# Kernel tuning notes

Measured on AMD Instinct MI355X. Metric: run time of the kernel, lower is better.

## Reference

```python
import jax, jax.numpy as jnp
import numpy as np

EPS_LN = 1e-5  # eqx.nn.LayerNorm default eps
DT_EPS = 1e-4  # softplus(dt) + 0.0001 in the module

H = 256  # hidden size
S = 256  # state size
B = 32
T = 4096


def setup_inputs() -> dict:
    key = jax.random.key(0)
    ks = jax.random.split(key, 8)
    sc = 1.0 / np.sqrt(H)
    return {
        "x": jax.random.normal(ks[0], (B, T, H), jnp.float32),
        "state0": jnp.zeros((B, S), jnp.float32),
        "in_to_state": jax.random.normal(ks[1], (S, H), jnp.float32) * sc,
        "state_to_hidden": jax.random.normal(ks[2], (H, S), jnp.float32) * sc,
        "direct": jax.random.normal(ks[3], (H,), jnp.float32) * sc,
        "a_diag": jax.random.normal(ks[4], (S,), jnp.float32),
        "g_diag": jax.random.normal(ks[5], (S,), jnp.float32),
        "dt": jax.random.normal(ks[6], (S,), jnp.float32) * 0.5 - 2.0,  # small timesteps
        "norm_w": jnp.ones((H,), jnp.float32),
        "norm_b": jnp.zeros((H,), jnp.float32),
        "out_w": jax.random.normal(ks[7], (H, H), jnp.float32) * sc,
        "out_b": jnp.zeros((H,), jnp.float32),
    }


def reference(x, state0, in_to_state, state_to_hidden, direct, a_diag, g_diag,
              dt, norm_w, norm_b, out_w, out_b):
    # Discretized diagonal oscillator coefficients (input-independent)
    dt_s = jax.nn.softplus(dt) + DT_EPS            # [S]
    omega = a_diag * dt_s                          # [S]
    decay = jnp.exp(-jax.nn.softplus(g_diag) * dt_s)
    decay = decay * decay                          # damped=True
    coeff = decay * jnp.cos(omega)                 # [S]

    # LayerNorm over feature dim (per-timestep, matching eqx.nn.LayerNorm)
    mu = jnp.mean(x, axis=-1, keepdims=True)
    var = jnp.var(x, axis=-1, keepdims=True)
    x_norm = (x - mu) * jax.lax.rsqrt(var + EPS_LN) * norm_w + norm_b  # [B,T,H]

    # Input injection: in_to_state @ x_norm for every timestep
    u = jnp.einsum("sh,bth->bts", in_to_state, x_norm)  # [B,T,S]

    # Diagonal linear recurrence: s_t = coeff * s_{t-1} + u_t
    def step(s, u_t):
        s = coeff * s + u_t
        return s, s

    u_t_major = jnp.swapaxes(u, 0, 1)                    # [T,B,S]
    final_state, states = jax.lax.scan(step, state0, u_t_major)
    states = jnp.swapaxes(states, 0, 1)                  # [B,T,S]

    # Readout + skip + gelu + out projection + residual
    mixed = jnp.einsum("hs,bts->bth", state_to_hidden, states) + direct * x_norm
    mixed = jax.nn.gelu(mixed)
    y = x + jnp.einsum("oh,bth->bto", out_w, mixed) + out_b
    return y, final_state
```

## Files before the change

kernel.cpp:

```cpp
#include <hip/hip_runtime.h>
#include <hip/hip_bf16.h>
#include <cstdint>
#include <cstddef>


typedef __bf16 bf16x8 __attribute__((ext_vector_type(8)));
typedef __bf16 bf16x4 __attribute__((ext_vector_type(4)));
typedef float  f32x4  __attribute__((ext_vector_type(4)));
typedef unsigned int u32x4 __attribute__((ext_vector_type(4)));

#define BB 32
#define TT 4096
#define HH 256
#define SS 256
#define MTOT (BB*TT)
#define NCHUNK 64
#define CLEN 64
#define NT 8

__global__ void prep_kernel(const float* __restrict__ w1, const float* __restrict__ w2,
                            const float* __restrict__ w3,
                            __bf16* __restrict__ w1b, __bf16* __restrict__ w2b,
                            __bf16* __restrict__ w3b,
                            const float* __restrict__ a_diag, const float* __restrict__ g_diag,
                            const float* __restrict__ dt,
                            float* __restrict__ coeff, float* __restrict__ cL) {
    int i = blockIdx.x * 256 + threadIdx.x;
    w1b[i] = (__bf16)w1[i];
    w2b[i] = (__bf16)w2[i];
    w3b[i] = (__bf16)w3[i];
    if (i < SS) {
        float d = dt[i];
        float sp = (d > 20.f) ? d : log1pf(expf(d));
        float dts = sp + 1e-4f;
        float omega = a_diag[i] * dts;
        float gg = g_diag[i];
        float spg = (gg > 20.f) ? gg : log1pf(expf(gg));
        float dec = expf(-spg * dts);
        float c = dec * dec * cosf(omega);
        coeff[i] = c;
        float p = c;
        #pragma unroll
        for (int q = 0; q < 6; ++q) p = p * p;
        cL[i] = p;
    }
}

__global__ __launch_bounds__(256) void ln_kernel(const float* __restrict__ x,
                          const float* __restrict__ w, const float* __restrict__ b,
                          __bf16* __restrict__ xn) {
    int row = blockIdx.x * 4 + (threadIdx.x >> 6);
    int lane = threadIdx.x & 63;
    size_t base = (size_t)row * HH + lane * 4;
    const float4 v = *(const float4*)&x[base];
    float s  = v.x + v.y + v.z + v.w;
    float ss = v.x*v.x + v.y*v.y + v.z*v.z + v.w*v.w;
    #pragma unroll
    for (int off = 32; off; off >>= 1) {
        s  += __shfl_xor(s,  off, 64);
        ss += __shfl_xor(ss, off, 64);
    }
    float mu  = s * (1.f/256.f);
    float var = ss * (1.f/256.f) - mu*mu;
    float sc  = rsqrtf(var + 1e-5f);
    const float4 wv = *(const float4*)&w[lane*4];
    const float4 bv = *(const float4*)&b[lane*4];
    union { __bf16 h[4]; uint2 u; } pk;
    pk.h[0] = (__bf16)((v.x - mu)*sc*wv.x + bv.x);
    pk.h[1] = (__bf16)((v.y - mu)*sc*wv.y + bv.y);
    pk.h[2] = (__bf16)((v.z - mu)*sc*wv.z + bv.z);
    pk.h[3] = (__bf16)((v.w - mu)*sc*wv.w + bv.w);
    *(uint2*)&xn[base] = pk.u;
}

template<int MODE>
__global__ __launch_bounds__(512, 2) void gemm_kernel(
    const __bf16* __restrict__ W,
    const __bf16* __restrict__ X,
    void* Cout,
    const __bf16* xn_in,
    const float* __restrict__ dvec,
    const float* __restrict__ xres,
    const float* __restrict__ bias)
{
    __shared__ __bf16 Xs[64 * 256];
    __shared__ __bf16 Es[64 * 256];

    const int tid  = threadIdx.x;
    const int lane = tid & 63;
    const int wid  = tid >> 6;
    const int l15  = lane & 15, quad = lane >> 4;
    const int wn   = wid >> 1;
    const int wm   = wid & 1;

    bf16x8 Wf[4][8];
    #pragma unroll
    for (int jn = 0; jn < 4; ++jn) {
        const int n = wn * 64 + jn * 16 + l15;
        #pragma unroll
        for (int kb = 0; kb < 8; ++kb)
            Wf[jn][kb] = *(const bf16x8*)&W[(size_t)n * 256 + kb * 32 + quad * 8];
    }

    int srow[4], scol[4], sdst[4];
    #pragma unroll
    for (int j = 0; j < 4; ++j) {
        int o = wid * 256 + j * 64 + lane;
        int m = o >> 5, g = o & 31;
        srow[j] = m;
        scol[j] = g * 8;
        sdst[j] = m * 512 + ((g ^ (m & 15)) * 16);
    }

    const size_t mbase = (size_t)blockIdx.x * (64 * NT);

    u32x4 pf[4];
    #pragma unroll
    for (int j = 0; j < 4; ++j)
        pf[j] = *(const u32x4*)&X[(mbase + srow[j]) * 256 + scol[j]];
    #pragma unroll
    for (int j = 0; j < 4; ++j)
        *(u32x4*)((char*)Xs + sdst[j]) = pf[j];
    __syncthreads();
    #pragma unroll
    for (int j = 0; j < 4; ++j)
        pf[j] = *(const u32x4*)&X[(mbase + 64 + srow[j]) * 256 + scol[j]];

    const int mrow0 = wm * 32 + l15;
    const int hrow  = tid >> 5;
    const int nc    = tid & 31;

    for (int it = 0; it < NT; ++it) {
        const size_t mt0 = mbase + (size_t)it * 64;

        f32x4 acc[2][4] = {};
        #pragma unroll
        for (int kb = 0; kb < 8; ++kb) {
            bf16x8 xf[2];
            #pragma unroll
            for (int im = 0; im < 2; ++im) {
                int m = mrow0 + im * 16;
                xf[im] = *(const bf16x8*)((char*)Xs + m * 512 + (((kb * 4 + quad) ^ l15) * 16));
            }
            #pragma unroll
            for (int jn = 0; jn < 4; ++jn)
                #pragma unroll
                for (int im = 0; im < 2; ++im)
                    acc[im][jn] = __builtin_amdgcn_mfma_f32_16x16x32_bf16(
                        Wf[jn][kb], xf[im], acc[im][jn], 0, 0, 0);
        }
        __syncthreads();

        if (it + 1 < NT) {
            #pragma unroll
            for (int j = 0; j < 4; ++j)
                *(u32x4*)((char*)Xs + sdst[j]) = pf[j];
        }
        #pragma unroll
        for (int im = 0; im < 2; ++im) {
            const int m = mrow0 + im * 16;
            #pragma unroll
            for (int jn = 0; jn < 4; ++jn) {
                const int gn = wn * 16 + jn * 4 + quad;
                bf16x4 pk;
                #pragma unroll
                for (int r = 0; r < 4; ++r) pk[r] = (__bf16)acc[im][jn][r];
                *(bf16x4*)((char*)Es + m * 512 + ((gn ^ (l15 << 2)) * 8)) = pk;
            }
        }
        __syncthreads();

        if (it + 2 < NT) {
            #pragma unroll
            for (int j = 0; j < 4; ++j)
                pf[j] = *(const u32x4*)&X[(mt0 + 128 + srow[j]) * 256 + scol[j]];
        }

        #pragma unroll
        for (int r = 0; r < 4; ++r) {
            const int m = r * 16 + hrow;
            bf16x8 ev = *(const bf16x8*)((char*)Es + m * 512 + (((nc * 2) ^ (hrow << 2)) * 8));
            const size_t gidx = (mt0 + m) * 256 + nc * 8;
            if (MODE == 0) {
                *(bf16x8*)((__bf16*)Cout + gidx) = ev;
            } else if (MODE == 1) {
                bf16x8 xv = *(const bf16x8*)&xn_in[gidx];
                f32x4 d0 = *(const f32x4*)&dvec[nc * 8];
                f32x4 d1 = *(const f32x4*)&dvec[nc * 8 + 4];
                bf16x8 pk;
                #pragma unroll
                for (int j = 0; j < 8; ++j) {
                    float dj = (j < 4) ? d0[j] : d1[j - 4];
                    float t = (float)ev[j] + dj * (float)xv[j];
                    float th = tanhf(0.7978845608028654f * (t + 0.044715f * t * t * t));
                    pk[j] = (__bf16)(0.5f * t * (1.0f + th));
                }
                *(bf16x8*)((__bf16*)Cout + gidx) = pk;
            } else {
                f32x4 x0 = *(const f32x4*)&xres[gidx];
                f32x4 x1 = *(const f32x4*)&xres[gidx + 4];
                f32x4 b0 = *(const f32x4*)&bias[nc * 8];
                f32x4 b1 = *(const f32x4*)&bias[nc * 8 + 4];
                f32x4 y0, y1;
                #pragma unroll
                for (int j = 0; j < 4; ++j) {
                    y0[j] = x0[j] + (float)ev[j]     + b0[j];
                    y1[j] = x1[j] + (float)ev[j + 4] + b1[j];
                }
                *(f32x4*)((float*)Cout + gidx)     = y0;
                *(f32x4*)((float*)Cout + gidx + 4) = y1;
            }
        }
    }
}

__global__ __launch_bounds__(256) void scan_carries(const __bf16* __restrict__ u,
                             const float* __restrict__ coeff,
                             const float* __restrict__ state0, float* __restrict__ carry) {
    int ch = blockIdx.x, b = blockIdx.y, s = threadIdx.x;
    float c = coeff[s];
    float st = (ch == 0) ? state0[b * SS + s] : 0.f;
    size_t base = ((size_t)b * TT + (size_t)ch * CLEN) * SS + s;
    #pragma unroll 8
    for (int i = 0; i < CLEN; ++i)
        st = c * st + (float)u[base + (size_t)i * SS];
    carry[(b * NCHUNK + ch) * SS + s] = st;
}

__global__ __launch_bounds__(256) void scan_prefix(float* carry, const float* __restrict__ cL,
                            float* __restrict__ fs_out) {
    int b = blockIdx.x, s = threadIdx.x;
    float cl = cL[s];
    float P = 0.f;
    for (int j = 0; j < NCHUNK; ++j) {
        int idx = (b * NCHUNK + j) * SS + s;
        P = cl * P + carry[idx];
        carry[idx] = P;
    }
    fs_out[b * SS + s] = P;
}

__global__ __launch_bounds__(256) void scan_apply(__bf16* u, const float* __restrict__ coeff,
                           const float* __restrict__ state0,
                           const float* __restrict__ carry) {
    int ch = blockIdx.x, b = blockIdx.y, s = threadIdx.x;
    float c = coeff[s];
    float st = (ch == 0) ? state0[b * SS + s]
                         : carry[(b * NCHUNK + ch - 1) * SS + s];
    size_t base = ((size_t)b * TT + (size_t)ch * CLEN) * SS + s;
    #pragma unroll 8
    for (int i = 0; i < CLEN; ++i) {
        st = c * st + (float)u[base + (size_t)i * SS];
        u[base + (size_t)i * SS] = (__bf16)st;
    }
}

extern "C" void kernel_launch(void* const* d_in, const int* in_sizes, int n_in,
                              void* d_out, int out_size, void* d_ws, size_t ws_size,
                              hipStream_t stream) {
    const float* x      = (const float*)d_in[0];
    const float* state0 = (const float*)d_in[1];
    const float* w1     = (const float*)d_in[2];
    const float* w2     = (const float*)d_in[3];
    const float* direct = (const float*)d_in[4];
    const float* a_diag = (const float*)d_in[5];
    const float* g_diag = (const float*)d_in[6];
    const float* dt     = (const float*)d_in[7];
    const float* norm_w = (const float*)d_in[8];
    const float* norm_b = (const float*)d_in[9];
    const float* w3     = (const float*)d_in[10];
    const float* out_b  = (const float*)d_in[11];

    char* ws = (char*)d_ws;
    const size_t MH2 = (size_t)MTOT * HH * 2;
    __bf16* xn    = (__bf16*)(ws);
    __bf16* u     = (__bf16*)(ws + MH2);
    __bf16* w1b   = (__bf16*)(ws + 2*MH2);
    __bf16* w2b   = (__bf16*)(ws + 2*MH2 + 131072);
    __bf16* w3b   = (__bf16*)(ws + 2*MH2 + 262144);
    float*  coeff = (float*)(ws + 2*MH2 + 393216);
    float*  cL    = (float*)(ws + 2*MH2 + 394240);
    float*  carry = (float*)(ws + 2*MH2 + 395264);

    float* y_out  = (float*)d_out;
    float* fs_out = (float*)d_out + (size_t)MTOT * HH;

    prep_kernel<<<256, 256, 0, stream>>>(w1, w2, w3, w1b, w2b, w3b,
                                         a_diag, g_diag, dt, coeff, cL);
    ln_kernel<<<MTOT/4, 256, 0, stream>>>(x, norm_w, norm_b, xn);
    gemm_kernel<0><<<256, 512, 0, stream>>>(w1b, xn, u, nullptr, nullptr, nullptr, nullptr);
    scan_carries<<<dim3(NCHUNK, BB), 256, 0, stream>>>(u, coeff, state0, carry);
    scan_prefix<<<BB, 256, 0, stream>>>(carry, cL, fs_out);
    scan_apply<<<dim3(NCHUNK, BB), 256, 0, stream>>>(u, coeff, state0, carry);
    gemm_kernel<1><<<256, 512, 0, stream>>>(w2b, u, xn, xn, direct, nullptr, nullptr);
    gemm_kernel<2><<<256, 512, 0, stream>>>(w3b, xn, y_out, nullptr, nullptr, x, out_b);
}
```

Measured before the change: 430.1 us.

## Fuse chunked scan carries and apply into the GEMM kernels

```diff
diff --git a/kernel.cpp b/kernel.cpp
--- a/kernel.cpp
+++ b/kernel.cpp
@@ -15,7 +15,6 @@
 #define SS 256
 #define MTOT (BB*TT)
 #define NCHUNK 64
-#define CLEN 64
 #define NT 8
 
 __global__ void prep_kernel(const float* __restrict__ w1, const float* __restrict__ w2,
@@ -73,77 +72,141 @@
     *(uint2*)&xn[base] = pk.u;
 }
 
+__device__ __forceinline__ void scan_xs_tile(__bf16* Xs, int tid, float c, float& st) {
+    const int gb = tid >> 3, bo = (tid & 7) << 1;
+    #pragma unroll
+    for (int g4 = 0; g4 < 4; ++g4) {
+        float v[8];
+        #pragma unroll
+        for (int r = 0; r < 8; ++r) {
+            const int m = g4 * 8 + r;
+            v[r] = (float)*(const __bf16*)((const char*)Xs + m * 512 + (((gb ^ (m & 15)) << 4) | bo));
+        }
+        __bf16 w[8];
+        #pragma unroll
+        for (int r = 0; r < 8; ++r) { st = c * st + v[r]; w[r] = (__bf16)st; }
+        #pragma unroll
+        for (int r = 0; r < 8; ++r) {
+            const int m = g4 * 8 + r;
+            *(__bf16*)((char*)Xs + m * 512 + (((gb ^ (m & 15)) << 4) | bo)) = w[r];
+        }
+    }
+}
+
+__device__ __forceinline__ void scan_es_carry(const __bf16* Es, int tid, float c, float& st) {
+    const int gb = tid >> 2, bo = (tid & 3) << 1;
+    #pragma unroll
+    for (int g4 = 0; g4 < 4; ++g4) {
+        float v[8];
+        #pragma unroll
+        for (int r = 0; r < 8; ++r) {
+            const int m = g4 * 8 + r;
+            v[r] = (float)*(const __bf16*)((const char*)Es + m * 512 + (((gb ^ ((m & 15) << 2)) << 3) | bo));
+        }
+        #pragma unroll
+        for (int r = 0; r < 8; ++r) st = c * st + v[r];
+    }
+}
+
 template<int MODE>
-__global__ __launch_bounds__(512, 2) void gemm_kernel(
+__global__ __launch_bounds__(512, 4) void gemm_kernel(
     const __bf16* __restrict__ W,
     const __bf16* __restrict__ X,
     void* Cout,
     const __bf16* xn_in,
     const float* __restrict__ dvec,
     const float* __restrict__ xres,
-    const float* __restrict__ bias)
+    const float* __restrict__ bias,
+    const float* __restrict__ coeff,
+    const float* __restrict__ state0,
+    float* carry)
 {
-    __shared__ __bf16 Xs[64 * 256];
-    __shared__ __bf16 Es[64 * 256];
+    __shared__ __bf16 Xs[32 * 256];
+    __shared__ __bf16 Es[32 * 256];
 
     const int tid  = threadIdx.x;
     const int lane = tid & 63;
     const int wid  = tid >> 6;
     const int l15  = lane & 15, quad = lane >> 4;
-    const int wn   = wid >> 1;
-    const int wm   = wid & 1;
-
-    bf16x8 Wf[4][8];
-    #pragma unroll
-    for (int jn = 0; jn < 4; ++jn) {
-        const int n = wn * 64 + jn * 16 + l15;
+
+    bf16x8 Wf[2][8];
+    #pragma unroll
+    for (int jn = 0; jn < 2; ++jn) {
+        const int n = wid * 32 + jn * 16 + l15;
         #pragma unroll
         for (int kb = 0; kb < 8; ++kb)
             Wf[jn][kb] = *(const bf16x8*)&W[(size_t)n * 256 + kb * 32 + quad * 8];
     }
 
-    int srow[4], scol[4], sdst[4];
-    #pragma unroll
-    for (int j = 0; j < 4; ++j) {
-        int o = wid * 256 + j * 64 + lane;
-        int m = o >> 5, g = o & 31;
+    const int bxi = blockIdx.x;
+    const int bb  = bxi >> 4;
+    const int chb = (bxi & 15) * 4;
+    float c_s = 0.f, s0v = 0.f, cin0 = 0.f, cin1 = 0.f, cin2 = 0.f, cin3 = 0.f;
+    if constexpr (MODE == 0) {
+        if (tid < 256) {
+            c_s = coeff[tid];
+            if (chb == 0) s0v = state0[(size_t)bb * 256 + tid];
+        }
+    }
+    if constexpr (MODE == 1) {
+        if (tid < 256) {
+            c_s = coeff[tid];
+            cin0 = (chb == 0) ? state0[(size_t)bb * 256 + tid]
+                              : carry[((size_t)bb * 64 + chb - 1) * 256 + tid];
+            cin1 = carry[((size_t)bb * 64 + chb + 0) * 256 + tid];
+            cin2 = carry[((size_t)bb * 64 + chb + 1) * 256 + tid];
+            cin3 = carry[((size_t)bb * 64 + chb + 2) * 256 + tid];
+        }
+    }
+
+    int sdst[2], srow[2];
+    const int g = tid & 31;
+    #pragma unroll
+    for (int j = 0; j < 2; ++j) {
+        const int m = j * 16 + (tid >> 5);
         srow[j] = m;
-        scol[j] = g * 8;
         sdst[j] = m * 512 + ((g ^ (m & 15)) * 16);
     }
-
-    const size_t mbase = (size_t)blockIdx.x * (64 * NT);
-
-    u32x4 pf[4];
-    #pragma unroll
-    for (int j = 0; j < 4; ++j)
-        pf[j] = *(const u32x4*)&X[(mbase + srow[j]) * 256 + scol[j]];
-    #pragma unroll
-    for (int j = 0; j < 4; ++j)
+    const int colb = g * 16;
+
+    const size_t mbase = (size_t)bxi * 256;
+    const char* Xb = (const char*)X;
+
+    u32x4 pf[2];
+    #pragma unroll
+    for (int j = 0; j < 2; ++j)
+        pf[j] = *(const u32x4*)(Xb + (mbase + srow[j]) * 512 + colb);
+    #pragma unroll
+    for (int j = 0; j < 2; ++j)
         *(u32x4*)((char*)Xs + sdst[j]) = pf[j];
     __syncthreads();
     #pragma unroll
-    for (int j = 0; j < 4; ++j)
-        pf[j] = *(const u32x4*)&X[(mbase + 64 + srow[j]) * 256 + scol[j]];
-
-    const int mrow0 = wm * 32 + l15;
-    const int hrow  = tid >> 5;
-    const int nc    = tid & 31;
+    for (int j = 0; j < 2; ++j)
+        pf[j] = *(const u32x4*)(Xb + (mbase + 32 + srow[j]) * 512 + colb);
+
+    float st  = 0.f;
+    float stc = 0.f;
+    if constexpr (MODE == 1) {
+        if (tid < 256) { st = cin0; scan_xs_tile(Xs, tid, c_s, st); }
+        __syncthreads();
+    }
+
+    const int hrow = tid >> 5;
+    const int nc   = tid & 31;
 
     for (int it = 0; it < NT; ++it) {
-        const size_t mt0 = mbase + (size_t)it * 64;
-
-        f32x4 acc[2][4] = {};
+        const size_t mt0 = mbase + (size_t)it * 32;
+
+        f32x4 acc[2][2] = {};
         #pragma unroll
         for (int kb = 0; kb < 8; ++kb) {
             bf16x8 xf[2];
             #pragma unroll
-            for (int im = 0; im < 2; ++im) {
-                int m = mrow0 + im * 16;
-                xf[im] = *(const bf16x8*)((char*)Xs + m * 512 + (((kb * 4 + quad) ^ l15) * 16));
-            }
-            #pragma unroll
-            for (int jn = 0; jn < 4; ++jn)
+            for (int im = 0; im < 2; ++im)
+                xf[im] = *(const bf16x8*)((const char*)Xs + (l15 + im * 16) * 512
+                                          + (((kb * 4 + quad) ^ l15) * 16));
+            #pragma unroll
+            for (int jn = 0; jn < 2; ++jn)
                 #pragma unroll
                 for (int im = 0; im < 2; ++im)
                     acc[im][jn] = __builtin_amdgcn_mfma_f32_16x16x32_bf16(
@@ -153,15 +216,15 @@
 
         if (it + 1 < NT) {
             #pragma unroll
-            for (int j = 0; j < 4; ++j)
+            for (int j = 0; j < 2; ++j)
                 *(u32x4*)((char*)Xs + sdst[j]) = pf[j];
         }
         #pragma unroll
         for (int im = 0; im < 2; ++im) {
-            const int m = mrow0 + im * 16;
-            #pragma unroll
-            for (int jn = 0; jn < 4; ++jn) {
-                const int gn = wn * 16 + jn * 4 + quad;
+            const int m = l15 + im * 16;
+            #pragma unroll
+            for (int jn = 0; jn < 2; ++jn) {
+                const int gn = wid * 8 + jn * 4 + quad;
                 bf16x4 pk;
                 #pragma unroll
                 for (int r = 0; r < 4; ++r) pk[r] = (__bf16)acc[im][jn][r];
@@ -172,14 +235,25 @@
 
         if (it + 2 < NT) {
             #pragma unroll
-            for (int j = 0; j < 4; ++j)
-                pf[j] = *(const u32x4*)&X[(mt0 + 128 + srow[j]) * 256 + scol[j]];
-        }
-
-        #pragma unroll
-        for (int r = 0; r < 4; ++r) {
+            for (int j = 0; j < 2; ++j)
+                pf[j] = *(const u32x4*)(Xb + (mt0 + 64 + srow[j]) * 512 + colb);
+        }
+
+        if constexpr (MODE == 1) {
+            if (it + 1 < NT && tid < 256) {
+                const int itt = it + 1;
+                if ((itt & 1) == 0) {
+                    const int k = itt >> 1;
+                    st = (k == 1) ? cin1 : (k == 2) ? cin2 : cin3;
+                }
+                scan_xs_tile(Xs, tid, c_s, st);
+            }
+        }
+
+        #pragma unroll
+        for (int r = 0; r < 2; ++r) {
             const int m = r * 16 + hrow;
-            bf16x8 ev = *(const bf16x8*)((char*)Es + m * 512 + (((nc * 2) ^ (hrow << 2)) * 8));
+            bf16x8 ev = *(const bf16x8*)((const char*)Es + m * 512 + (((nc * 2) ^ (hrow << 2)) * 8));
             const size_t gidx = (mt0 + m) * 256 + nc * 8;
             if (MODE == 0) {
                 *(bf16x8*)((__bf16*)Cout + gidx) = ev;
@@ -192,8 +266,9 @@
                 for (int j = 0; j < 8; ++j) {
                     float dj = (j < 4) ? d0[j] : d1[j - 4];
                     float t = (float)ev[j] + dj * (float)xv[j];
-                    float th = tanhf(0.7978845608028654f * (t + 0.044715f * t * t * t));
-                    pk[j] = (__bf16)(0.5f * t * (1.0f + th));
+                    float q = t + 0.044715f * t * t * t;
+                    float e = __expf(-1.5957691216057308f * q);
+                    pk[j] = (__bf16)(t * __builtin_amdgcn_rcpf(1.f + e));
                 }
                 *(bf16x8*)((__bf16*)Cout + gidx) = pk;
             } else {
@@ -211,20 +286,20 @@
                 *(f32x4*)((float*)Cout + gidx + 4) = y1;
             }
         }
-    }
-}
-
-__global__ __launch_bounds__(256) void scan_carries(const __bf16* __restrict__ u,
-                             const float* __restrict__ coeff,
-                             const float* __restrict__ state0, float* __restrict__ carry) {
-    int ch = blockIdx.x, b = blockIdx.y, s = threadIdx.x;
-    float c = coeff[s];
-    float st = (ch == 0) ? state0[b * SS + s] : 0.f;
-    size_t base = ((size_t)b * TT + (size_t)ch * CLEN) * SS + s;
-    #pragma unroll 8
-    for (int i = 0; i < CLEN; ++i)
-        st = c * st + (float)u[base + (size_t)i * SS];
-    carry[(b * NCHUNK + ch) * SS + s] = st;
+
+        if constexpr (MODE == 0) {
+            if (tid < 256) {
+                if ((it & 1) == 0) stc = (it == 0 && chb == 0) ? s0v : 0.f;
+                scan_es_carry(Es, tid, c_s, stc);
+                if ((it & 1) == 1)
+                    carry[((size_t)bb * 64 + (chb + (it >> 1))) * 256 + tid] = stc;
+            }
+        }
+
+        if constexpr (MODE == 1) {
+            if (it + 1 < NT) __syncthreads();
+        }
+    }
 }
 
 __global__ __launch_bounds__(256) void scan_prefix(float* carry, const float* __restrict__ cL,
@@ -238,21 +313,6 @@
         carry[idx] = P;
     }
     fs_out[b * SS + s] = P;
-}
-
-__global__ __launch_bounds__(256) void scan_apply(__bf16* u, const float* __restrict__ coeff,
-                           const float* __restrict__ state0,
-                           const float* __restrict__ carry) {
-    int ch = blockIdx.x, b = blockIdx.y, s = threadIdx.x;
-    float c = coeff[s];
-    float st = (ch == 0) ? state0[b * SS + s]
-                         : carry[(b * NCHUNK + ch - 1) * SS + s];
-    size_t base = ((size_t)b * TT + (size_t)ch * CLEN) * SS + s;
-    #pragma unroll 8
-    for (int i = 0; i < CLEN; ++i) {
-        st = c * st + (float)u[base + (size_t)i * SS];
-        u[base + (size_t)i * SS] = (__bf16)st;
-    }
 }
 
 extern "C" void kernel_launch(void* const* d_in, const int* in_sizes, int n_in,
@@ -288,10 +348,11 @@
     prep_kernel<<<256, 256, 0, stream>>>(w1, w2, w3, w1b, w2b, w3b,
                                          a_diag, g_diag, dt, coeff, cL);
     ln_kernel<<<MTOT/4, 256, 0, stream>>>(x, norm_w, norm_b, xn);
-    gemm_kernel<0><<<256, 512, 0, stream>>>(w1b, xn, u, nullptr, nullptr, nullptr, nullptr);
-    scan_carries<<<dim3(NCHUNK, BB), 256, 0, stream>>>(u, coeff, state0, carry);
+    gemm_kernel<0><<<512, 512, 0, stream>>>(w1b, xn, u, nullptr, nullptr, nullptr, nullptr,
+                                            coeff, state0, carry);
     scan_prefix<<<BB, 256, 0, stream>>>(carry, cL, fs_out);
-    scan_apply<<<dim3(NCHUNK, BB), 256, 0, stream>>>(u, coeff, state0, carry);
-    gemm_kernel<1><<<256, 512, 0, stream>>>(w2b, u, xn, xn, direct, nullptr, nullptr);
-    gemm_kernel<2><<<256, 512, 0, stream>>>(w3b, xn, y_out, nullptr, nullptr, x, out_b);
-}
+    gemm_kernel<1><<<512, 512, 0, stream>>>(w2b, u, xn, xn, direct, nullptr, nullptr,
+                                            coeff, state0, carry);
+    gemm_kernel<2><<<512, 512, 0, stream>>>(w3b, xn, y_out, nullptr, nullptr, x, out_b,
+                                            nullptr, nullptr, nullptr);
+}
```

Result: no change. 434.9 us (+1.1%).
